# Kernel optimization log

Measured on AMD Instinct MI355X. Metric: run time of the kernel, lower is better.

The kernel has to match this reference:

```python
import jax, jax.numpy as jnp
import numpy as np

NUM_HEADS = 16
CHUNK = 128


def _bitlinear(x, w, b):
    # BitLinear 1.58b: ternary weights + int8 activations with STE (forward value is exact quantized math)
    w_scale = jnp.maximum(jnp.mean(jnp.abs(w)), 1e-5)
    w_norm = w / w_scale
    w_q = jax.lax.stop_gradient(jnp.sign(w_norm) - w_norm) + w_norm
    x_scale = jnp.maximum(jnp.max(jnp.abs(x), axis=-1, keepdims=True), 1e-5)
    x_norm = x / x_scale * 127.0
    x_q = jax.lax.stop_gradient(jnp.round(x_norm) - x_norm) + x_norm
    return jnp.einsum('...i,oi->...o', x_q, w_q) * (x_scale * w_scale / 127.0) + b


def _rmsnorm(x, w, eps=1e-6):
    return x * jax.lax.rsqrt(jnp.mean(x * x, axis=-1, keepdims=True) + eps) * w


def setup_inputs():
    key = jax.random.key(0)
    ks = jax.random.split(key, 8)
    B, N, C = 2, 4096, 2048
    def w(k, shape):
        return jax.random.normal(k, shape, jnp.float32) * 0.02
    return {
        'x': jax.random.normal(ks[0], (B, N, C), jnp.float32),
        'qkv_w': w(ks[1], (3 * C, C)), 'qkv_b': w(ks[2], (3 * C,)),
        'gate_w': w(ks[3], (C, C)), 'gate_b': w(ks[4], (C,)),
        'proj_w': w(ks[5], (C, C)), 'proj_b': w(ks[6], (C,)),
        'norm_w': jnp.ones((C,), jnp.float32),
    }


def reference(x, qkv_w, qkv_b, gate_w, gate_b, proj_w, proj_b, norm_w):
    B, N, C = x.shape
    H, L = NUM_HEADS, CHUNK
    D = C // H
    scale = D ** -0.5
    qkv = _bitlinear(x, qkv_w, qkv_b).reshape(B, N, 3, H, D)
    q, k, v = qkv[:, :, 0], qkv[:, :, 1], qkv[:, :, 2]
    g = jax.nn.sigmoid(_bitlinear(x, gate_w, gate_b)).reshape(B, N, H, D)
    nc = N // L  # N chosen as multiple of chunk_size -> pad branch is a no-op

    def chunks(t):  # (B,N,H,D) -> (nc,B,L,H,D) for scan over chunks
        return t.reshape(B, nc, L, H, D).transpose(1, 0, 2, 3, 4)
    qc, kc, vc, gc = map(chunks, (q, k, v, g))

    def step(kv_state, inp):
        qi, ki, vi, gi = inp  # each (B,L,H,D)
        # faithful to torch: qi @ ki.transpose(-2,-1) contracts head_dim per position -> (B,L,H,H)
        attn = jax.nn.softmax(jnp.einsum('blhd,blgd->blhg', qi, ki) * scale, axis=-1)
        local = jnp.einsum('blhg,blgd->blhd', attn, vi)
        recur = jnp.einsum('blhd,bhde->blhe', qi, kv_state)
        decay = jnp.mean(gi, axis=1)[..., None]          # (B,H,D,1)
        kv_update = jnp.einsum('blhd,blhe->bhde', ki, vi)
        return kv_state * decay + kv_update, local + recur

    kv0 = jnp.zeros((B, H, D, D), x.dtype)
    _, out = jax.lax.scan(step, kv0, (qc, kc, vc, gc))  # out: (nc,B,L,H,D)
    out = out.transpose(1, 0, 2, 3, 4).reshape(B, N, C)
    return _bitlinear(_rmsnorm(out, norm_w), proj_w, proj_b)
```

## Files before the change

kernel.cpp:

```cpp
#include <hip/hip_runtime.h>
#include <stdint.h>

typedef __attribute__((ext_vector_type(4))) float f32x4;
typedef __attribute__((ext_vector_type(8))) __bf16 bf16x8;
typedef __attribute__((ext_vector_type(4))) unsigned int u32x4;
typedef __attribute__((ext_vector_type(4))) int i32x4;

#define DEV static __device__ __forceinline__

DEV float bf2f(unsigned short h){ union{unsigned int u; float f;} v; v.u=((unsigned int)h)<<16; return v.f; }
DEV unsigned short f2bf(float f){ union{float ff; unsigned int u;} v; v.ff=f; unsigned int u=v.u;
  u += 0x7fffu + ((u>>16)&1u); return (unsigned short)(u>>16); }

DEV f32x4 mfma16(bf16x8 a, bf16x8 b, f32x4 c){
  return __builtin_amdgcn_mfma_f32_16x16x32_bf16(a, b, c, 0, 0, 0);
}
DEV i32x4 mfma_i8(i32x4 a, i32x4 b, i32x4 c){
  return __builtin_amdgcn_mfma_i32_16x16x64_i8(a, b, c, 0, 0, 0);
}

#define GLOAD_LDS16(gptr, ldsptr) \
  __builtin_amdgcn_global_load_lds( \
      (const __attribute__((address_space(1))) unsigned int*)(gptr), \
      (__attribute__((address_space(3))) unsigned int*)(ldsptr), 16, 0, 0)

__global__ __launch_bounds__(256) void k_quant_w(
    const float* __restrict__ wq, const float* __restrict__ wg, const float* __restrict__ wp,
    signed char* __restrict__ oq, signed char* __restrict__ og, signed char* __restrict__ op,
    float* __restrict__ partials)
{
  int blk = blockIdx.x, t = threadIdx.x;
  const float* src; signed char* dst; long base;
  if (blk < 3072){ src=wq; dst=oq; base=(long)blk*4096; }
  else if (blk < 4096){ src=wg; dst=og; base=(long)(blk-3072)*4096; }
  else { src=wp; dst=op; base=(long)(blk-4096)*4096; }
  float s = 0.f;
  #pragma unroll
  for (int i=0;i<4;i++){
    long e = base + (long)(i*256 + t)*4;
    float4 v = *reinterpret_cast<const float4*>(src + e);
    s += fabsf(v.x)+fabsf(v.y)+fabsf(v.z)+fabsf(v.w);
    signed char tmp[4];
    tmp[0] = (v.x>0.f)?1:((v.x<0.f)?-1:0);
    tmp[1] = (v.y>0.f)?1:((v.y<0.f)?-1:0);
    tmp[2] = (v.z>0.f)?1:((v.z<0.f)?-1:0);
    tmp[3] = (v.w>0.f)?1:((v.w<0.f)?-1:0);
    *reinterpret_cast<unsigned int*>(dst + e) = *reinterpret_cast<unsigned int*>(tmp);
  }
  #pragma unroll
  for (int m=1;m<64;m<<=1) s += __shfl_xor(s, m);
  __shared__ float red[4];
  if ((t&63)==0) red[t>>6]=s;
  __syncthreads();
  if (t==0) partials[blk] = red[0]+red[1]+red[2]+red[3];
}

__global__ void k_finalize(const float* __restrict__ partials, float* __restrict__ scales)
{
  int t = threadIdx.x;
  __shared__ float red[4];
  for (int w=0; w<3; w++){
    int s0 = (w==0)?0:((w==1)?3072:4096);
    int s1 = (w==0)?3072:((w==1)?4096:5120);
    float acc = 0.f;
    for (int i=s0+t; i<s1; i+=256) acc += partials[i];
    #pragma unroll
    for (int m=1;m<64;m<<=1) acc += __shfl_xor(acc, m);
    if ((t&63)==0) red[t>>6]=acc;
    __syncthreads();
    if (t==0){
      float total = red[0]+red[1]+red[2]+red[3];
      float denom = (w==0)? 12582912.0f : 4194304.0f;
      float wsc = fmaxf(total/denom, 1e-5f);
      scales[w] = wsc / 127.0f;
    }
    __syncthreads();
  }
}

__global__ __launch_bounds__(256) void k_quant_x(const float* __restrict__ x,
    signed char* __restrict__ xq, float* __restrict__ xs)
{
  int row=blockIdx.x, t=threadIdx.x;
  const float* xr = x + (long)row*2048;
  float v[8];
  float4 a = *reinterpret_cast<const float4*>(xr + t*8);
  float4 b = *reinterpret_cast<const float4*>(xr + t*8 + 4);
  v[0]=a.x; v[1]=a.y; v[2]=a.z; v[3]=a.w; v[4]=b.x; v[5]=b.y; v[6]=b.z; v[7]=b.w;
  float mx=0.f;
  #pragma unroll
  for (int j=0;j<8;j++) mx = fmaxf(mx, fabsf(v[j]));
  #pragma unroll
  for (int m=1;m<64;m<<=1) mx = fmaxf(mx, __shfl_xor(mx, m));
  __shared__ float red[4];
  if ((t&63)==0) red[t>>6]=mx;
  __syncthreads();
  float sc = fmaxf(fmaxf(fmaxf(red[0],red[1]),fmaxf(red[2],red[3])), 1e-5f);
  if (t==0) xs[row]=sc;
  signed char q[8];
  #pragma unroll
  for (int j=0;j<8;j++) q[j] = (signed char)(int)rintf((v[j]/sc)*127.f);
  *reinterpret_cast<uint2*>(xq + (long)row*2048 + t*8) = *reinterpret_cast<uint2*>(q);
}

template<int MODE, int NBN>
__global__ __launch_bounds__(256) void k_gemm(
    const signed char* __restrict__ A, const signed char* __restrict__ Bw,
    const float* __restrict__ xs, const float* __restrict__ scales,
    const float* __restrict__ bias0, const float* __restrict__ bias1,
    unsigned short* __restrict__ oq, unsigned short* __restrict__ ok, unsigned short* __restrict__ ov,
    float* __restrict__ decay, float* __restrict__ of32)
{
  __shared__ signed char As[2][128*128];
  __shared__ signed char Bs[2][128*128];
  const int K = 2048, NT = 16;
  int tid=threadIdx.x;
  const int nwg = NBN*64, cpx = nwg>>3;
  int wg  = ((int)blockIdx.x & 7)*cpx + ((int)blockIdx.x >> 3);
  int super = wg >> 6, inner = wg & 63;
  int bn = (super % (NBN>>3))*8 + (inner & 7);
  int bm = (super / (NBN>>3))*8 + (inner >> 3);
  long n0=(long)bn*128, m0=(long)bm*128;
  int wave=tid>>6, lane=tid&63, l15=lane&15, l4=lane>>4;
  int wr=wave>>1, wc=wave&1;
  int srow = wave*8 + (lane>>3);
  int scol = ((lane&7) ^ ((lane>>3)&7))*16;
  i32x4 z4 = {0,0,0,0};
  i32x4 acc[4][4];
  #pragma unroll
  for (int i=0;i<4;i++)
    #pragma unroll
    for (int j=0;j<4;j++) acc[i][j]=z4;

#define STAGE_ALL(buf, kt) do{ \
    GLOAD_LDS16(A  + (m0 +  0 + srow)*K + (kt) + scol, &As[buf][(  0 + wave*8)*128]); \
    GLOAD_LDS16(A  + (m0 + 32 + srow)*K + (kt) + scol, &As[buf][( 32 + wave*8)*128]); \
    GLOAD_LDS16(A  + (m0 + 64 + srow)*K + (kt) + scol, &As[buf][( 64 + wave*8)*128]); \
    GLOAD_LDS16(A  + (m0 + 96 + srow)*K + (kt) + scol, &As[buf][( 96 + wave*8)*128]); \
    GLOAD_LDS16(Bw + (n0 +  0 + srow)*K + (kt) + scol, &Bs[buf][(  0 + wave*8)*128]); \
    GLOAD_LDS16(Bw + (n0 + 32 + srow)*K + (kt) + scol, &Bs[buf][( 32 + wave*8)*128]); \
    GLOAD_LDS16(Bw + (n0 + 64 + srow)*K + (kt) + scol, &Bs[buf][( 64 + wave*8)*128]); \
    GLOAD_LDS16(Bw + (n0 + 96 + srow)*K + (kt) + scol, &Bs[buf][( 96 + wave*8)*128]); }while(0)
#define RD_A(buf, mr, kk) (*reinterpret_cast<const i32x4*>(&As[buf][(wr*64+(mr)*16+l15)*128 + ((((kk)*4+l4) ^ (l15&7))<<4)]))
#define RD_B(buf, nr, kk) (*reinterpret_cast<const i32x4*>(&Bs[buf][(wc*64+(nr)*16+l15)*128 + ((((kk)*4+l4) ^ (l15&7))<<4)]))

  STAGE_ALL(0, 0);

  for (int t=0; t<NT; ++t){
    int c = t&1;
    if (t+1 < NT){
      STAGE_ALL(c^1, (t+1)*128);
      asm volatile("s_waitcnt vmcnt(8)" ::: "memory");
    } else {
      asm volatile("s_waitcnt vmcnt(0)" ::: "memory");
    }
    __builtin_amdgcn_s_barrier();
    __builtin_amdgcn_s_setprio(1);
    #pragma unroll
    for (int kk=0;kk<2;kk++){
      i32x4 af[4], bfr[4];
      #pragma unroll
      for (int mr=0;mr<4;mr++) af[mr] = RD_A(c,mr,kk);
      #pragma unroll
      for (int nr=0;nr<4;nr++) bfr[nr] = RD_B(c,nr,kk);
      #pragma unroll
      for (int mr=0;mr<4;mr++)
        #pragma unroll
        for (int nr=0;nr<4;nr++)
          acc[mr][nr] = mfma_i8(af[mr], bfr[nr], acc[mr][nr]);
    }
    __builtin_amdgcn_s_setprio(0);
    if (t+1 < NT) __builtin_amdgcn_s_barrier();
  }

  if (MODE==0 && bn < 48){
    float fac = scales[0];
    float xsv[4][4];
    #pragma unroll
    for (int mr=0;mr<4;mr++)
      #pragma unroll
      for (int r2=0;r2<4;r2++)
        xsv[mr][r2] = xs[m0 + wr*64 + mr*16 + 4*l4 + r2] * fac;
    int sidx = (int)(n0 >> 11);
    unsigned short* dst = (sidx==0)?oq:((sidx==1)?ok:ov);
    int c0 = (int)(n0 & 2047);
    #pragma unroll
    for (int nr=0;nr<4;nr++){
      int c = c0 + wc*64 + nr*16 + l15;
      float bv = bias0[n0 + wc*64 + nr*16 + l15];
      #pragma unroll
      for (int mr=0;mr<4;mr++)
        #pragma unroll
        for (int r2=0;r2<4;r2++){
          long grow = m0 + wr*64 + mr*16 + 4*l4 + r2;
          dst[grow*2048 + c] = f2bf((float)acc[mr][nr][r2]*xsv[mr][r2] + bv);
        }
    }
  } else if (MODE==0){
    int bng = bn - 48;
    float fac = scales[1];
    float xsv[4][4];
    #pragma unroll
    for (int mr=0;mr<4;mr++)
      #pragma unroll
      for (int r2=0;r2<4;r2++)
        xsv[mr][r2] = xs[m0 + wr*64 + mr*16 + 4*l4 + r2] * fac;
    float* red = reinterpret_cast<float*>(As);
    #pragma unroll
    for (int nr=0;nr<4;nr++){
      float bv = bias1[bng*128 + wc*64 + nr*16 + l15];
      float ssum = 0.f;
      #pragma unroll
      for (int mr=0;mr<4;mr++)
        #pragma unroll
        for (int r2=0;r2<4;r2++){
          float val = (float)acc[mr][nr][r2]*xsv[mr][r2] + bv;
          ssum += 1.f/(1.f + expf(-val));
        }
      ssum += __shfl_xor(ssum, 16);
      ssum += __shfl_xor(ssum, 32);
      if (l4==0) red[wr*128 + wc*64 + nr*16 + l15] = ssum;
    }
    __syncthreads();
    if (tid < 128){
      float d = (red[tid] + red[128+tid]) * (1.0f/128.0f);
      decay[((long)bm*16 + bng)*128 + tid] = d;
    }
  } else {
    float fac = scales[2];
    float xsv[4][4];
    #pragma unroll
    for (int mr=0;mr<4;mr++)
      #pragma unroll
      for (int r2=0;r2<4;r2++)
        xsv[mr][r2] = xs[m0 + wr*64 + mr*16 + 4*l4 + r2] * fac;
    #pragma unroll
    for (int nr=0;nr<4;nr++){
      long c = n0 + wc*64 + nr*16 + l15;
      float bv = bias0[c];
      #pragma unroll
      for (int mr=0;mr<4;mr++)
        #pragma unroll
        for (int r2=0;r2<4;r2++){
          long grow = m0 + wr*64 + mr*16 + 4*l4 + r2;
          of32[grow*2048 + c] = (float)acc[mr][nr][r2]*xsv[mr][r2] + bv;
        }
    }
  }
#undef STAGE_ALL
#undef RD_A
#undef RD_B
}

__global__ __launch_bounds__(256) void k_attnA(const unsigned short* __restrict__ qb,
    const unsigned short* __restrict__ kb, const unsigned short* __restrict__ vb,
    unsigned short* __restrict__ aof)
{
  __shared__ unsigned short at[4][16*32];
  __shared__ unsigned short vT[4][128*40];
  int tid=threadIdx.x, wave=tid>>6, lane=tid&63, l15=lane&15, l4=lane>>4;
  const float SCALE = 0.08838834764831845f;

  for (int i=lane;i<16*32;i+=64) at[wave][i]=0;
  for (int i=lane;i<128*40;i+=64) vT[wave][i]=0;

  long token = (long)blockIdx.x*4 + wave;
  long base = token*2048;

  bf16x8 qf[4], kf[4];
  #pragma unroll
  for (int kk=0;kk<4;kk++){
    qf[kk] = *reinterpret_cast<const bf16x8*>(qb + base + l15*128 + kk*32 + l4*8);
    kf[kk] = *reinterpret_cast<const bf16x8*>(kb + base + l15*128 + kk*32 + l4*8);
  }
  {
    int g = lane>>2, e0 = (lane&3)*32;
    #pragma unroll
    for (int j=0;j<4;j++){
      u32x4 vv = *reinterpret_cast<const u32x4*>(vb + base + g*128 + e0 + j*8);
      unsigned short tmp[8];
      *reinterpret_cast<u32x4*>(tmp) = vv;
      #pragma unroll
      for (int t2=0;t2<8;t2++) vT[wave][(e0+j*8+t2)*40 + g] = tmp[t2];
    }
  }

  f32x4 s = {0.f,0.f,0.f,0.f};
  #pragma unroll
  for (int kk=0;kk<4;kk++) s = mfma16(qf[kk], kf[kk], s);

  #pragma unroll
  for (int r2=0;r2<4;r2++){
    float v = s[r2];
    float m = v;
    m = fmaxf(m, __shfl_xor(m,1)); m = fmaxf(m, __shfl_xor(m,2));
    m = fmaxf(m, __shfl_xor(m,4)); m = fmaxf(m, __shfl_xor(m,8));
    float p = expf((v-m)*SCALE);
    float sum = p;
    sum += __shfl_xor(sum,1); sum += __shfl_xor(sum,2);
    sum += __shfl_xor(sum,4); sum += __shfl_xor(sum,8);
    at[wave][(4*l4+r2)*32 + l15] = f2bf(p/sum);
  }
  __syncthreads();

  bf16x8 pa = *reinterpret_cast<const bf16x8*>(&at[wave][l15*32 + l4*8]);
  #pragma unroll
  for (int eb=0;eb<8;eb++){
    bf16x8 vf = *reinterpret_cast<const bf16x8*>(&vT[wave][(eb*16+l15)*40 + l4*8]);
    f32x4 z4 = {0.f,0.f,0.f,0.f};
    f32x4 o = mfma16(pa, vf, z4);
    #pragma unroll
    for (int r2=0;r2<4;r2++)
      aof[base + (long)(4*l4+r2)*128 + eb*16 + l15] = f2bf(o[r2]);
  }
}

__global__ __launch_bounds__(256) void k_updB1(
    const unsigned short* __restrict__ kb, const unsigned short* __restrict__ vb,
    float* __restrict__ upds)
{
  __shared__ unsigned short kT[128*128];
  __shared__ unsigned short vT[128*128];
  int bid=blockIdx.x;
  int ch = bid&31, h=(bid>>5)&15, b=bid>>9;
  int tid=threadIdx.x, wave=tid>>6, lane=tid&63, l15=lane&15, l4=lane>>4;
  long base = ((long)b*4096 + (long)ch*128)*2048 + h*128;

  #pragma unroll
  for (int i=0;i<8;i++){
    int s = tid + i*256;
    int l = s>>4, sl = s&15;
    unsigned short tmp[8];
    u32x4 v1 = *reinterpret_cast<const u32x4*>(kb + base + (long)l*2048 + sl*8);
    *reinterpret_cast<u32x4*>(tmp) = v1;
    #pragma unroll
    for (int j=0;j<8;j++){
      int d = sl*8+j;
      kT[d*128 + (((l>>3)^(d&15))<<3) + (l&7)] = tmp[j];
    }
    u32x4 v2 = *reinterpret_cast<const u32x4*>(vb + base + (long)l*2048 + sl*8);
    *reinterpret_cast<u32x4*>(tmp) = v2;
    #pragma unroll
    for (int j=0;j<8;j++){
      int e = sl*8+j;
      vT[e*128 + (((l>>3)^(e&15))<<3) + (l&7)] = tmp[j];
    }
  }
  __syncthreads();

  f32x4 z4 = {0.f,0.f,0.f,0.f};
  f32x4 acc[2][8];
  #pragma unroll
  for (int er=0;er<2;er++)
    #pragma unroll
    for (int dc=0;dc<8;dc++) acc[er][dc]=z4;

  #pragma unroll
  for (int kk=0;kk<4;kk++){
    bf16x8 xf[2];
    #pragma unroll
    for (int er=0;er<2;er++){
      int e = wave*32 + er*16 + l15;
      xf[er] = *reinterpret_cast<const bf16x8*>(vT + e*128 + (((kk*4+l4)^(e&15))<<3));
    }
    #pragma unroll
    for (int dc=0;dc<8;dc++){
      int d = dc*16 + l15;
      bf16x8 kf = *reinterpret_cast<const bf16x8*>(kT + d*128 + (((kk*4+l4)^(d&15))<<3));
      #pragma unroll
      for (int er=0;er<2;er++)
        acc[er][dc] = mfma16(xf[er], kf, acc[er][dc]);
    }
  }

  float* dst = upds + (long)bid*16384;
  #pragma unroll
  for (int er=0;er<2;er++)
    #pragma unroll
    for (int dc=0;dc<8;dc++)
      #pragma unroll
      for (int r2=0;r2<4;r2++){
        int e = wave*32 + er*16 + 4*l4 + r2;
        int d = dc*16 + l15;
        dst[e*128 + d] = acc[er][dc][r2];
      }
}

__global__ __launch_bounds__(256) void k_scanB2(float* __restrict__ buf,
    const float* __restrict__ decay)
{
  int bid=blockIdx.x;
  int strip = bid&7, bh = bid>>3;
  int b = bh>>4, h = bh&15;
  int t = threadIdx.x;
  int f0 = t, f1 = t + 256;
  int e0 = strip*16 + (f0>>5), d0 = (f0&31)*4;
  int e1 = strip*16 + (f1>>5);
  long base = (long)bh * 32 * 16384;
  long o0 = (long)e0*128 + d0;
  long o1 = (long)e1*128 + d0;
  float4 s0 = {0.f,0.f,0.f,0.f}, s1 = {0.f,0.f,0.f,0.f};
  for (int ch=0; ch<32; ch++){
    float* p = buf + base + (long)ch*16384;
    float4 u0 = *reinterpret_cast<float4*>(p + o0);
    float4 u1 = *reinterpret_cast<float4*>(p + o1);
    *reinterpret_cast<float4*>(p + o0) = s0;
    *reinterpret_cast<float4*>(p + o1) = s1;
    float4 dc = *reinterpret_cast<const float4*>(decay + ((long)(b*32+ch)*16 + h)*128 + d0);
    s0.x = s0.x*dc.x + u0.x; s0.y = s0.y*dc.y + u0.y;
    s0.z = s0.z*dc.z + u0.z; s0.w = s0.w*dc.w + u0.w;
    s1.x = s1.x*dc.x + u1.x; s1.y = s1.y*dc.y + u1.y;
    s1.z = s1.z*dc.z + u1.z; s1.w = s1.w*dc.w + u1.w;
  }
}

__global__ __launch_bounds__(256) void k_recurB3(
    const unsigned short* __restrict__ qb, const float* __restrict__ upds,
    unsigned short* __restrict__ aof)
{
  __shared__ unsigned short sh[128*128];
  __shared__ unsigned short slo[128*128];
  int bid=blockIdx.x;
  int ch = bid&31, h=(bid>>5)&15, b=bid>>9;
  int tid=threadIdx.x, wave=tid>>6, lane=tid&63, l15=lane&15, l4=lane>>4;
  long slab = (long)bid*16384;
  long base = ((long)b*4096 + (long)ch*128)*2048 + h*128;

  #pragma unroll
  for (int i=0;i<8;i++){
    int s = tid + i*256;
    int e = s>>4, sl = s&15;
    float4 a = *reinterpret_cast<const float4*>(upds + slab + (long)e*128 + sl*8);
    float4 c = *reinterpret_cast<const float4*>(upds + slab + (long)e*128 + sl*8 + 4);
    float vv[8] = {a.x,a.y,a.z,a.w,c.x,c.y,c.z,c.w};
    unsigned short hi[8], lo[8];
    #pragma unroll
    for (int j=0;j<8;j++){
      hi[j] = f2bf(vv[j]);
      lo[j] = f2bf(vv[j] - bf2f(hi[j]));
    }
    int slot = e*128 + ((sl ^ (e&15))<<3);
    *reinterpret_cast<u32x4*>(sh + slot)  = *reinterpret_cast<u32x4*>(hi);
    *reinterpret_cast<u32x4*>(slo + slot) = *reinterpret_cast<u32x4*>(lo);
  }

  bf16x8 qf[2][4];
  #pragma unroll
  for (int mr=0;mr<2;mr++)
    #pragma unroll
    for (int kk=0;kk<4;kk++)
      qf[mr][kk] = *reinterpret_cast<const bf16x8*>(qb + base + (long)(wave*32+mr*16+l15)*2048 + kk*32 + l4*8);
  __syncthreads();

  f32x4 z4 = {0.f,0.f,0.f,0.f};
  f32x4 acc[2][8];
  #pragma unroll
  for (int mr=0;mr<2;mr++)
    #pragma unroll
    for (int ec=0;ec<8;ec++) acc[mr][ec]=z4;

  #pragma unroll
  for (int kk=0;kk<4;kk++)
    #pragma unroll
    for (int ec=0;ec<8;ec++){
      int e = ec*16 + l15;
      int slot = (((kk*4+l4)^(e&15))<<3);
      bf16x8 tfh = *reinterpret_cast<const bf16x8*>(sh + e*128 + slot);
      bf16x8 tfl = *reinterpret_cast<const bf16x8*>(slo + e*128 + slot);
      #pragma unroll
      for (int mr=0;mr<2;mr++){
        acc[mr][ec] = mfma16(qf[mr][kk], tfh, acc[mr][ec]);
        acc[mr][ec] = mfma16(qf[mr][kk], tfl, acc[mr][ec]);
      }
    }

  #pragma unroll
  for (int mr=0;mr<2;mr++)
    #pragma unroll
    for (int ec=0;ec<8;ec++)
      #pragma unroll
      for (int r2=0;r2<4;r2++){
        long o = base + (long)(wave*32+mr*16+4*l4+r2)*2048 + ec*16 + l15;
        aof[o] = f2bf(bf2f(aof[o]) + acc[mr][ec][r2]);
      }
}

__global__ __launch_bounds__(256) void k_rmsnorm_quant(const unsigned short* __restrict__ ain,
    const float* __restrict__ normw, signed char* __restrict__ x2q, float* __restrict__ xs2)
{
  int row=blockIdx.x, t=threadIdx.x;
  const unsigned short* rp = ain + (long)row*2048;
  u32x4 raw = *reinterpret_cast<const u32x4*>(rp + t*8);
  unsigned short tmp[8];
  *reinterpret_cast<u32x4*>(tmp) = raw;
  float xv[8]; float ss=0.f;
  #pragma unroll
  for (int j=0;j<8;j++){ xv[j]=bf2f(tmp[j]); ss += xv[j]*xv[j]; }
  #pragma unroll
  for (int m=1;m<64;m<<=1) ss += __shfl_xor(ss, m);
  __shared__ float red[4];
  if ((t&63)==0) red[t>>6]=ss;
  __syncthreads();
  float ms = (red[0]+red[1]+red[2]+red[3])*(1.0f/2048.0f) + 1e-6f;
  float rs = 1.0f/sqrtf(ms);
  __syncthreads();
  float4 w0 = *reinterpret_cast<const float4*>(normw + t*8);
  float4 w1 = *reinterpret_cast<const float4*>(normw + t*8 + 4);
  float wv[8] = {w0.x,w0.y,w0.z,w0.w,w1.x,w1.y,w1.z,w1.w};
  float y[8]; float mx=0.f;
  #pragma unroll
  for (int j=0;j<8;j++){ y[j] = xv[j]*rs*wv[j]; mx = fmaxf(mx, fabsf(y[j])); }
  #pragma unroll
  for (int m=1;m<64;m<<=1) mx = fmaxf(mx, __shfl_xor(mx, m));
  __shared__ float red2[4];
  if ((t&63)==0) red2[t>>6]=mx;
  __syncthreads();
  float sc = fmaxf(fmaxf(fmaxf(red2[0],red2[1]),fmaxf(red2[2],red2[3])), 1e-5f);
  if (t==0) xs2[row]=sc;
  signed char q[8];
  #pragma unroll
  for (int j=0;j<8;j++) q[j] = (signed char)(int)rintf((y[j]/sc)*127.f);
  *reinterpret_cast<uint2*>(x2q + (long)row*2048 + t*8) = *reinterpret_cast<uint2*>(q);
}

extern "C" void kernel_launch(void* const* d_in, const int* in_sizes, int n_in,
                              void* d_out, int out_size, void* d_ws, size_t ws_size,
                              hipStream_t stream)
{
  const float* x      = (const float*)d_in[0];
  const float* qkv_w  = (const float*)d_in[1];
  const float* qkv_b  = (const float*)d_in[2];
  const float* gate_w = (const float*)d_in[3];
  const float* gate_b = (const float*)d_in[4];
  const float* proj_w = (const float*)d_in[5];
  const float* proj_b = (const float*)d_in[6];
  const float* norm_w = (const float*)d_in[7];
  (void)in_sizes; (void)n_in; (void)out_size; (void)ws_size;

  char* ws = (char*)d_ws;
  const size_t MB = 1024UL*1024UL;
  signed char* wq_proj = (signed char*)(ws + 0*MB);
  signed char* wq_qkv  = (signed char*)(ws + 4*MB);
  signed char* wq_gate = (signed char*)(ws + 16*MB);
  signed char* xq      = (signed char*)(ws + 20*MB);
  float*       upds    = (float*)(ws + 4*MB);
  unsigned short* qb   = (unsigned short*)(ws + 68*MB);
  unsigned short* kb   = (unsigned short*)(ws + 100*MB);
  unsigned short* vb   = (unsigned short*)(ws + 132*MB);
  unsigned short* aof  = (unsigned short*)(ws + 164*MB);
  signed char* x2q     = (signed char*)qb;
  float* xs       = (float*)(ws + 196*MB);
  float* xs2      = xs + 8192;
  float* decay    = xs2 + 8192;
  float* partials = decay + 131072;
  float* scales   = partials + 5120;

  k_quant_w<<<5120,256,0,stream>>>(qkv_w, gate_w, proj_w, wq_qkv, wq_gate, wq_proj, partials);
  k_finalize<<<1,256,0,stream>>>(partials, scales);
  k_quant_x<<<8192,256,0,stream>>>(x, xq, xs);
  k_gemm<0,64><<<4096,256,0,stream>>>(xq, wq_qkv, xs, scales, qkv_b, gate_b,
      qb,kb,vb, decay, nullptr);
  k_attnA<<<2048,256,0,stream>>>(qb,kb,vb, aof);
  k_updB1<<<1024,256,0,stream>>>(kb, vb, upds);
  k_scanB2<<<256,256,0,stream>>>(upds, decay);
  k_recurB3<<<1024,256,0,stream>>>(qb, upds, aof);
  k_rmsnorm_quant<<<8192,256,0,stream>>>(aof, norm_w, x2q, xs2);
  k_gemm<2,16><<<1024,256,0,stream>>>(x2q, wq_proj, xs2, scales, proj_b, nullptr,
      nullptr,nullptr,nullptr, nullptr, (float*)d_out);
}
```

Baseline: 395.1 us.

## Enlarge int8 GEMM tiles to 256x256 with 512-thread workgroups

The int8 MFMA GEMM moves from 128x128 tiles with 4 waves to 256x256 tiles with 8 waves, each wave computing a 128x64 sub-tile. Staging, swizzle and epilogue indexing are rewritten to match. The gate epilogue now writes the per-chunk decay means directly from each wave instead of reducing across waves through shared memory. Larger tiles raise arithmetic intensity and halve global traffic per FLOP. The cost is 128KB of LDS and one workgroup per CU, and the proj GEMM launches only 256 workgroups, which may underfill the GPU.

```diff
diff --git a/kernel.cpp b/kernel.cpp
--- a/kernel.cpp
+++ b/kernel.cpp
@@ -104,45 +104,45 @@
 }
 
 template<int MODE, int NBN>
-__global__ __launch_bounds__(256) void k_gemm(
+__global__ __launch_bounds__(512, 1) void k_gemm(
     const signed char* __restrict__ A, const signed char* __restrict__ Bw,
     const float* __restrict__ xs, const float* __restrict__ scales,
     const float* __restrict__ bias0, const float* __restrict__ bias1,
     unsigned short* __restrict__ oq, unsigned short* __restrict__ ok, unsigned short* __restrict__ ov,
     float* __restrict__ decay, float* __restrict__ of32)
 {
-  __shared__ signed char As[2][128*128];
-  __shared__ signed char Bs[2][128*128];
+  __shared__ signed char As[2][256*128];
+  __shared__ signed char Bs[2][256*128];
   const int K = 2048, NT = 16;
   int tid=threadIdx.x;
-  const int nwg = NBN*64, cpx = nwg>>3;
+  const int nwg = NBN*32, cpx = nwg>>3;
   int wg  = ((int)blockIdx.x & 7)*cpx + ((int)blockIdx.x >> 3);
   int super = wg >> 6, inner = wg & 63;
   int bn = (super % (NBN>>3))*8 + (inner & 7);
   int bm = (super / (NBN>>3))*8 + (inner >> 3);
-  long n0=(long)bn*128, m0=(long)bm*128;
+  long n0=(long)bn*256, m0=(long)bm*256;
   int wave=tid>>6, lane=tid&63, l15=lane&15, l4=lane>>4;
-  int wr=wave>>1, wc=wave&1;
-  int srow = wave*8 + (lane>>3);
-  int scol = ((lane&7) ^ ((lane>>3)&7))*16;
+  int wm=wave>>2, wn=wave&3;
+  int srow = wave*32 + (lane>>3);
+  int scol = ((lane&7) ^ (lane>>3))*16;
   i32x4 z4 = {0,0,0,0};
-  i32x4 acc[4][4];
-  #pragma unroll
-  for (int i=0;i<4;i++)
+  i32x4 acc[8][4];
+  #pragma unroll
+  for (int i=0;i<8;i++)
     #pragma unroll
     for (int j=0;j<4;j++) acc[i][j]=z4;
 
 #define STAGE_ALL(buf, kt) do{ \
-    GLOAD_LDS16(A  + (m0 +  0 + srow)*K + (kt) + scol, &As[buf][(  0 + wave*8)*128]); \
-    GLOAD_LDS16(A  + (m0 + 32 + srow)*K + (kt) + scol, &As[buf][( 32 + wave*8)*128]); \
-    GLOAD_LDS16(A  + (m0 + 64 + srow)*K + (kt) + scol, &As[buf][( 64 + wave*8)*128]); \
-    GLOAD_LDS16(A  + (m0 + 96 + srow)*K + (kt) + scol, &As[buf][( 96 + wave*8)*128]); \
-    GLOAD_LDS16(Bw + (n0 +  0 + srow)*K + (kt) + scol, &Bs[buf][(  0 + wave*8)*128]); \
-    GLOAD_LDS16(Bw + (n0 + 32 + srow)*K + (kt) + scol, &Bs[buf][( 32 + wave*8)*128]); \
-    GLOAD_LDS16(Bw + (n0 + 64 + srow)*K + (kt) + scol, &Bs[buf][( 64 + wave*8)*128]); \
-    GLOAD_LDS16(Bw + (n0 + 96 + srow)*K + (kt) + scol, &Bs[buf][( 96 + wave*8)*128]); }while(0)
-#define RD_A(buf, mr, kk) (*reinterpret_cast<const i32x4*>(&As[buf][(wr*64+(mr)*16+l15)*128 + ((((kk)*4+l4) ^ (l15&7))<<4)]))
-#define RD_B(buf, nr, kk) (*reinterpret_cast<const i32x4*>(&Bs[buf][(wc*64+(nr)*16+l15)*128 + ((((kk)*4+l4) ^ (l15&7))<<4)]))
+    GLOAD_LDS16(A  + (m0 + srow +  0)*K + (kt) + scol, &As[buf][(wave*32 +  0)*128]); \
+    GLOAD_LDS16(A  + (m0 + srow +  8)*K + (kt) + scol, &As[buf][(wave*32 +  8)*128]); \
+    GLOAD_LDS16(A  + (m0 + srow + 16)*K + (kt) + scol, &As[buf][(wave*32 + 16)*128]); \
+    GLOAD_LDS16(A  + (m0 + srow + 24)*K + (kt) + scol, &As[buf][(wave*32 + 24)*128]); \
+    GLOAD_LDS16(Bw + (n0 + srow +  0)*K + (kt) + scol, &Bs[buf][(wave*32 +  0)*128]); \
+    GLOAD_LDS16(Bw + (n0 + srow +  8)*K + (kt) + scol, &Bs[buf][(wave*32 +  8)*128]); \
+    GLOAD_LDS16(Bw + (n0 + srow + 16)*K + (kt) + scol, &Bs[buf][(wave*32 + 16)*128]); \
+    GLOAD_LDS16(Bw + (n0 + srow + 24)*K + (kt) + scol, &Bs[buf][(wave*32 + 24)*128]); }while(0)
+#define RD_A(buf, mi, kk) (*reinterpret_cast<const i32x4*>(&As[buf][(wm*128+(mi)*16+l15)*128 + ((((kk)*4+l4) ^ (l15&7))<<4)]))
+#define RD_B(buf, ni, kk) (*reinterpret_cast<const i32x4*>(&Bs[buf][(wn*64 +(ni)*16+l15)*128 + ((((kk)*4+l4) ^ (l15&7))<<4)]))
 
   STAGE_ALL(0, 0);
 
@@ -158,92 +158,92 @@
     __builtin_amdgcn_s_setprio(1);
     #pragma unroll
     for (int kk=0;kk<2;kk++){
-      i32x4 af[4], bfr[4];
-      #pragma unroll
-      for (int mr=0;mr<4;mr++) af[mr] = RD_A(c,mr,kk);
-      #pragma unroll
-      for (int nr=0;nr<4;nr++) bfr[nr] = RD_B(c,nr,kk);
-      #pragma unroll
-      for (int mr=0;mr<4;mr++)
+      i32x4 af[8], bfr[4];
+      #pragma unroll
+      for (int mi=0;mi<8;mi++) af[mi] = RD_A(c,mi,kk);
+      #pragma unroll
+      for (int ni=0;ni<4;ni++) bfr[ni] = RD_B(c,ni,kk);
+      #pragma unroll
+      for (int mi=0;mi<8;mi++)
         #pragma unroll
-        for (int nr=0;nr<4;nr++)
-          acc[mr][nr] = mfma_i8(af[mr], bfr[nr], acc[mr][nr]);
+        for (int ni=0;ni<4;ni++)
+          acc[mi][ni] = mfma_i8(af[mi], bfr[ni], acc[mi][ni]);
     }
     __builtin_amdgcn_s_setprio(0);
     if (t+1 < NT) __builtin_amdgcn_s_barrier();
   }
 
-  if (MODE==0 && bn < 48){
+  if (MODE==0 && bn < 24){
     float fac = scales[0];
-    float xsv[4][4];
-    #pragma unroll
-    for (int mr=0;mr<4;mr++)
+    float xsv[8][4];
+    #pragma unroll
+    for (int mi=0;mi<8;mi++)
       #pragma unroll
       for (int r2=0;r2<4;r2++)
-        xsv[mr][r2] = xs[m0 + wr*64 + mr*16 + 4*l4 + r2] * fac;
+        xsv[mi][r2] = xs[m0 + wm*128 + mi*16 + 4*l4 + r2] * fac;
     int sidx = (int)(n0 >> 11);
     unsigned short* dst = (sidx==0)?oq:((sidx==1)?ok:ov);
     int c0 = (int)(n0 & 2047);
     #pragma unroll
-    for (int nr=0;nr<4;nr++){
-      int c = c0 + wc*64 + nr*16 + l15;
-      float bv = bias0[n0 + wc*64 + nr*16 + l15];
-      #pragma unroll
-      for (int mr=0;mr<4;mr++)
+    for (int ni=0;ni<4;ni++){
+      int c = c0 + wn*64 + ni*16 + l15;
+      float bv = bias0[n0 + wn*64 + ni*16 + l15];
+      #pragma unroll
+      for (int mi=0;mi<8;mi++)
         #pragma unroll
         for (int r2=0;r2<4;r2++){
-          long grow = m0 + wr*64 + mr*16 + 4*l4 + r2;
-          dst[grow*2048 + c] = f2bf((float)acc[mr][nr][r2]*xsv[mr][r2] + bv);
+          long grow = m0 + wm*128 + mi*16 + 4*l4 + r2;
+          dst[grow*2048 + c] = f2bf((float)acc[mi][ni][r2]*xsv[mi][r2] + bv);
         }
     }
   } else if (MODE==0){
-    int bng = bn - 48;
     float fac = scales[1];
-    float xsv[4][4];
-    #pragma unroll
-    for (int mr=0;mr<4;mr++)
+    float xsv[8][4];
+    #pragma unroll
+    for (int mi=0;mi<8;mi++)
       #pragma unroll
       for (int r2=0;r2<4;r2++)
-        xsv[mr][r2] = xs[m0 + wr*64 + mr*16 + 4*l4 + r2] * fac;
-    float* red = reinterpret_cast<float*>(As);
-    #pragma unroll
-    for (int nr=0;nr<4;nr++){
-      float bv = bias1[bng*128 + wc*64 + nr*16 + l15];
+        xsv[mi][r2] = xs[m0 + wm*128 + mi*16 + 4*l4 + r2] * fac;
+    long row0 = m0 + wm*128;
+    int b = (int)(row0>>12), ch = (int)((row0>>7)&31);
+    #pragma unroll
+    for (int ni=0;ni<4;ni++){
+      long cg = n0 + wn*64 + ni*16 + l15;
+      long g = cg - 6144;
+      float bv = bias1[g];
       float ssum = 0.f;
       #pragma unroll
-      for (int mr=0;mr<4;mr++)
+      for (int mi=0;mi<8;mi++)
         #pragma unroll
         for (int r2=0;r2<4;r2++){
-          float val = (float)acc[mr][nr][r2]*xsv[mr][r2] + bv;
+          float val = (float)acc[mi][ni][r2]*xsv[mi][r2] + bv;
           ssum += 1.f/(1.f + expf(-val));
         }
       ssum += __shfl_xor(ssum, 16);
       ssum += __shfl_xor(ssum, 32);
-      if (l4==0) red[wr*128 + wc*64 + nr*16 + l15] = ssum;
-    }
-    __syncthreads();
-    if (tid < 128){
-      float d = (red[tid] + red[128+tid]) * (1.0f/128.0f);
-      decay[((long)bm*16 + bng)*128 + tid] = d;
+      if (l4==0){
+        int h = (int)(g>>7), d = (int)(g&127);
+        decay[((long)(b*32+ch)*16 + h)*128 + d] = ssum*(1.0f/128.0f);
+      }
     }
   } else {
     float fac = scales[2];
-    float xsv[4][4];
-    #pragma unroll
-    for (int mr=0;mr<4;mr++)
+    float xsv[8][4];
+    #pragma unroll
+    for (int mi=0;mi<8;mi++)
       #pragma unroll
       for (int r2=0;r2<4;r2++)
-        xsv[mr][r2] = xs[m0 + wr*64 + mr*16 + 4*l4 + r2] * fac;
-    #pragma unroll
-    for (int nr=0;nr<4;nr++){
-      long c = n0 + wc*64 + nr*16 + l15;
+        xsv[mi][r2] = xs[m0 + wm*128 + mi*16 + 4*l4 + r2] * fac;
+    #pragma unroll
+    for (int ni=0;ni<4;ni++){
+      long c = n0 + wn*64 + ni*16 + l15;
       float bv = bias0[c];
       #pragma unroll
-      for (int mr=0;mr<4;mr++)
+      for (int mi=0;mi<8;mi++)
         #pragma unroll
         for (int r2=0;r2<4;r2++){
-          long grow = m0 + wr*64 + mr*16 + 4*l4 + r2;
-          of32[grow*2048 + c] = (float)acc[mr][nr][r2]*xsv[mr][r2] + bv;
+          long grow = m0 + wm*128 + mi*16 + 4*l4 + r2;
+          of32[grow*2048 + c] = (float)acc[mi][ni][r2]*xsv[mi][r2] + bv;
         }
     }
   }
@@ -558,13 +558,13 @@
   k_quant_w<<<5120,256,0,stream>>>(qkv_w, gate_w, proj_w, wq_qkv, wq_gate, wq_proj, partials);
   k_finalize<<<1,256,0,stream>>>(partials, scales);
   k_quant_x<<<8192,256,0,stream>>>(x, xq, xs);
-  k_gemm<0,64><<<4096,256,0,stream>>>(xq, wq_qkv, xs, scales, qkv_b, gate_b,
+  k_gemm<0,32><<<1024,512,0,stream>>>(xq, wq_qkv, xs, scales, qkv_b, gate_b,
       qb,kb,vb, decay, nullptr);
   k_attnA<<<2048,256,0,stream>>>(qb,kb,vb, aof);
   k_updB1<<<1024,256,0,stream>>>(kb, vb, upds);
   k_scanB2<<<256,256,0,stream>>>(upds, decay);
   k_recurB3<<<1024,256,0,stream>>>(qb, upds, aof);
   k_rmsnorm_quant<<<8192,256,0,stream>>>(aof, norm_w, x2q, xs2);
-  k_gemm<2,16><<<1024,256,0,stream>>>(x2q, wq_proj, xs2, scales, proj_b, nullptr,
+  k_gemm<2,8><<<256,512,0,stream>>>(x2q, wq_proj, xs2, scales, proj_b, nullptr,
       nullptr,nullptr,nullptr, nullptr, (float*)d_out);
 }
```

Measured after the change: 404.4 us. +2.4%, slower.

## Switch int8 GEMM to three-stage pipeline with 64-wide K tiles

Applied to the files above, without the earlier changes.

The int8 GEMM K tile is halved from 128 to 64 and the LDS ring grows from two buffers to three, so loads run two tiles ahead. LDS per block drops from 64KB to 48KB, and launch bounds now request 3 blocks per SM to raise occupancy. The staging pattern and the XOR swizzle are reworked for 64-byte rows. The cost is twice as many barriers per K loop and less MFMA work between them. The 16-byte swizzle over 64-byte rows may also cause more LDS bank conflicts.

```diff
diff --git a/kernel.cpp b/kernel.cpp
--- a/kernel.cpp
+++ b/kernel.cpp
@@ -104,16 +104,16 @@
 }
 
 template<int MODE, int NBN>
-__global__ __launch_bounds__(256) void k_gemm(
+__global__ __launch_bounds__(256, 3) void k_gemm(
     const signed char* __restrict__ A, const signed char* __restrict__ Bw,
     const float* __restrict__ xs, const float* __restrict__ scales,
     const float* __restrict__ bias0, const float* __restrict__ bias1,
     unsigned short* __restrict__ oq, unsigned short* __restrict__ ok, unsigned short* __restrict__ ov,
     float* __restrict__ decay, float* __restrict__ of32)
 {
-  __shared__ signed char As[2][128*128];
-  __shared__ signed char Bs[2][128*128];
-  const int K = 2048, NT = 16;
+  __shared__ signed char As[3][128*64];
+  __shared__ signed char Bs[3][128*64];
+  const int K = 2048, NT = 32;
   int tid=threadIdx.x;
   const int nwg = NBN*64, cpx = nwg>>3;
   int wg  = ((int)blockIdx.x & 7)*cpx + ((int)blockIdx.x >> 3);
@@ -123,8 +123,8 @@
   long n0=(long)bn*128, m0=(long)bm*128;
   int wave=tid>>6, lane=tid&63, l15=lane&15, l4=lane>>4;
   int wr=wave>>1, wc=wave&1;
-  int srow = wave*8 + (lane>>3);
-  int scol = ((lane&7) ^ ((lane>>3)&7))*16;
+  int srow = wave*32 + (lane>>2);
+  int scol = ((lane&3) ^ ((lane>>2)&3))*16;
   i32x4 z4 = {0,0,0,0};
   i32x4 acc[4][4];
   #pragma unroll
@@ -133,36 +133,35 @@
     for (int j=0;j<4;j++) acc[i][j]=z4;
 
 #define STAGE_ALL(buf, kt) do{ \
-    GLOAD_LDS16(A  + (m0 +  0 + srow)*K + (kt) + scol, &As[buf][(  0 + wave*8)*128]); \
-    GLOAD_LDS16(A  + (m0 + 32 + srow)*K + (kt) + scol, &As[buf][( 32 + wave*8)*128]); \
-    GLOAD_LDS16(A  + (m0 + 64 + srow)*K + (kt) + scol, &As[buf][( 64 + wave*8)*128]); \
-    GLOAD_LDS16(A  + (m0 + 96 + srow)*K + (kt) + scol, &As[buf][( 96 + wave*8)*128]); \
-    GLOAD_LDS16(Bw + (n0 +  0 + srow)*K + (kt) + scol, &Bs[buf][(  0 + wave*8)*128]); \
-    GLOAD_LDS16(Bw + (n0 + 32 + srow)*K + (kt) + scol, &Bs[buf][( 32 + wave*8)*128]); \
-    GLOAD_LDS16(Bw + (n0 + 64 + srow)*K + (kt) + scol, &Bs[buf][( 64 + wave*8)*128]); \
-    GLOAD_LDS16(Bw + (n0 + 96 + srow)*K + (kt) + scol, &Bs[buf][( 96 + wave*8)*128]); }while(0)
-#define RD_A(buf, mr, kk) (*reinterpret_cast<const i32x4*>(&As[buf][(wr*64+(mr)*16+l15)*128 + ((((kk)*4+l4) ^ (l15&7))<<4)]))
-#define RD_B(buf, nr, kk) (*reinterpret_cast<const i32x4*>(&Bs[buf][(wc*64+(nr)*16+l15)*128 + ((((kk)*4+l4) ^ (l15&7))<<4)]))
+    GLOAD_LDS16(A  + (m0 + srow +  0)*K + (kt) + scol, &As[buf][(wave*32 +  0)*64]); \
+    GLOAD_LDS16(A  + (m0 + srow + 16)*K + (kt) + scol, &As[buf][(wave*32 + 16)*64]); \
+    GLOAD_LDS16(Bw + (n0 + srow +  0)*K + (kt) + scol, &Bs[buf][(wave*32 +  0)*64]); \
+    GLOAD_LDS16(Bw + (n0 + srow + 16)*K + (kt) + scol, &Bs[buf][(wave*32 + 16)*64]); }while(0)
+#define RD_A(buf, mr) (*reinterpret_cast<const i32x4*>(&As[buf][(wr*64+(mr)*16+l15)*64 + ((l4 ^ (l15&3))<<4)]))
+#define RD_B(buf, nr) (*reinterpret_cast<const i32x4*>(&Bs[buf][(wc*64+(nr)*16+l15)*64 + ((l4 ^ (l15&3))<<4)]))
 
   STAGE_ALL(0, 0);
-
+  STAGE_ALL(1, 64);
+
+  int c = 0;
   for (int t=0; t<NT; ++t){
-    int c = t&1;
-    if (t+1 < NT){
-      STAGE_ALL(c^1, (t+1)*128);
+    if (t+2 < NT){
+      int cn = c+2; if (cn>=3) cn-=3;
+      STAGE_ALL(cn, (t+2)*64);
       asm volatile("s_waitcnt vmcnt(8)" ::: "memory");
+    } else if (t+1 < NT){
+      asm volatile("s_waitcnt vmcnt(4)" ::: "memory");
     } else {
       asm volatile("s_waitcnt vmcnt(0)" ::: "memory");
     }
     __builtin_amdgcn_s_barrier();
     __builtin_amdgcn_s_setprio(1);
-    #pragma unroll
-    for (int kk=0;kk<2;kk++){
+    {
       i32x4 af[4], bfr[4];
       #pragma unroll
-      for (int mr=0;mr<4;mr++) af[mr] = RD_A(c,mr,kk);
-      #pragma unroll
-      for (int nr=0;nr<4;nr++) bfr[nr] = RD_B(c,nr,kk);
+      for (int mr=0;mr<4;mr++) af[mr] = RD_A(c,mr);
+      #pragma unroll
+      for (int nr=0;nr<4;nr++) bfr[nr] = RD_B(c,nr);
       #pragma unroll
       for (int mr=0;mr<4;mr++)
         #pragma unroll
@@ -171,6 +170,7 @@
     }
     __builtin_amdgcn_s_setprio(0);
     if (t+1 < NT) __builtin_amdgcn_s_barrier();
+    c = (c+1==3)?0:c+1;
   }
 
   if (MODE==0 && bn < 48){
@@ -186,14 +186,14 @@
     int c0 = (int)(n0 & 2047);
     #pragma unroll
     for (int nr=0;nr<4;nr++){
-      int c = c0 + wc*64 + nr*16 + l15;
+      int cc = c0 + wc*64 + nr*16 + l15;
       float bv = bias0[n0 + wc*64 + nr*16 + l15];
       #pragma unroll
       for (int mr=0;mr<4;mr++)
         #pragma unroll
         for (int r2=0;r2<4;r2++){
           long grow = m0 + wr*64 + mr*16 + 4*l4 + r2;
-          dst[grow*2048 + c] = f2bf((float)acc[mr][nr][r2]*xsv[mr][r2] + bv);
+          dst[grow*2048 + cc] = f2bf((float)acc[mr][nr][r2]*xsv[mr][r2] + bv);
         }
     }
   } else if (MODE==0){
@@ -236,14 +236,14 @@
         xsv[mr][r2] = xs[m0 + wr*64 + mr*16 + 4*l4 + r2] * fac;
     #pragma unroll
     for (int nr=0;nr<4;nr++){
-      long c = n0 + wc*64 + nr*16 + l15;
-      float bv = bias0[c];
+      long cc = n0 + wc*64 + nr*16 + l15;
+      float bv = bias0[cc];
       #pragma unroll
       for (int mr=0;mr<4;mr++)
         #pragma unroll
         for (int r2=0;r2<4;r2++){
           long grow = m0 + wr*64 + mr*16 + 4*l4 + r2;
-          of32[grow*2048 + c] = (float)acc[mr][nr][r2]*xsv[mr][r2] + bv;
+          of32[grow*2048 + cc] = (float)acc[mr][nr][r2]*xsv[mr][r2] + bv;
         }
     }
   }
```

Measured after the change: 402.0 us. Within noise of the previous version (+1.7%).
